# Optimization experiments

Measured on AMD Instinct MI355X. Metric: run time of the kernel, lower is better.

The kernel has to match this reference:

```python
import jax, jax.numpy as jnp
import numpy as np

DIM = 1024
EPS = 1e-5

def layernorm(x, g, b):
    m = jnp.mean(x, axis=-1, keepdims=True)
    v = jnp.var(x, axis=-1, keepdims=True)
    return (x - m) / jnp.sqrt(v + EPS) * g + b

def setup_inputs() -> dict:
    key = jax.random.key(0)
    ks = jax.random.split(key, 12)
    B, L, D = 4, 2048, DIM
    s = 1.0 / np.sqrt(D)
    return {
        "q": jax.random.normal(ks[0], (B, L, D), jnp.float32),
        "k": jax.random.normal(ks[1], (B, L, D), jnp.float32),
        "v": jax.random.normal(ks[2], (B, L, D), jnp.float32),
        "gq": jnp.ones((D,), jnp.float32), "bq": jnp.zeros((D,), jnp.float32),
        "gk": jnp.ones((D,), jnp.float32), "bk": jnp.zeros((D,), jnp.float32),
        "gv": jnp.ones((D,), jnp.float32), "bv": jnp.zeros((D,), jnp.float32),
        "Wq": jax.random.uniform(ks[3], (D, D), jnp.float32, -s, s),
        "Wk": jax.random.uniform(ks[4], (D, D), jnp.float32, -s, s),
        "Wv": jax.random.uniform(ks[5], (D, D), jnp.float32, -s, s),
        "Wp": jax.random.uniform(ks[6], (D, D), jnp.float32, -s, s),
        "bp": jax.random.uniform(ks[7], (D,), jnp.float32, -s, s),
    }

def reference(q, k, v, gq, bq, gk, bk, gv, bv, Wq, Wk, Wv, Wp, bp):
    scale = DIM ** -0.5
    qn = layernorm(q, gq, bq) @ Wq.T  # [B,Q,D]
    kn = layernorm(k, gk, bk) @ Wk.T  # [B,K,D]
    vn = layernorm(v, gv, bv) @ Wv.T  # [B,K,D]
    attn = jnp.einsum('bqc,bkc->bqk', qn, kn)
    attn = jax.nn.relu(attn) * scale  # ReLU on raw scores, then scale (matches in-place *=)
    attn_mask = jax.nn.softmax(attn, axis=-1)
    out = jnp.einsum('bqk,bkc->bqc', attn_mask, vn)
    out = out @ Wp.T + bp
    return (attn, out)
```

## Files before the change

kernel.cpp:

```cpp
#include <hip/hip_runtime.h>


typedef __attribute__((ext_vector_type(8))) short short8v;
typedef __attribute__((ext_vector_type(4))) float f32x4;

#define DEVI __device__ __forceinline__

DEVI float b2f(unsigned short u) {
  union { unsigned int i; float f; } x;
  x.i = ((unsigned int)u) << 16;
  return x.f;
}
DEVI unsigned short f2b(float f) {
  union { float f; unsigned int i; } x;
  x.f = f;
  unsigned int r = x.i + 0x7fffu + ((x.i >> 16) & 1u);
  return (unsigned short)(r >> 16);
}

DEVI bool sniff_bf16(const unsigned short* wq) {
  int bad = 0;
#pragma unroll
  for (int j = 0; j < 64; ++j) bad |= (fabsf(b2f(wq[j])) > 0.0625f) ? 1 : 0;
  return bad == 0;
}

DEVI void async16(const unsigned short* g, unsigned short* l) {
  __builtin_amdgcn_global_load_lds(
      (const __attribute__((address_space(1))) void*)g,
      (__attribute__((address_space(3))) void*)l, 16, 0, 0);
}

DEVI void wait_lgkm0() { asm volatile("s_waitcnt lgkmcnt(0)" ::: "memory"); }
template <int N> DEVI void wait_vm();
template <> DEVI void wait_vm<0>() { asm volatile("s_waitcnt vmcnt(0)" ::: "memory"); }
template <> DEVI void wait_vm<6>() { asm volatile("s_waitcnt vmcnt(6)" ::: "memory"); }
template <> DEVI void wait_vm<8>() { asm volatile("s_waitcnt vmcnt(8)" ::: "memory"); }

DEVI void stage_q(const unsigned short* G, int ld, unsigned short* L,
                  int w, int lane, int k0) {
  int r8 = lane >> 3;
  int scol = ((lane & 7) ^ r8) * 8;
  async16(G + (size_t)(w * 8 + r8) * ld + k0 + scol, L + (w * 8) * 64);
}
DEVI void stage_half(const unsigned short* G, int ld, unsigned short* L,
                     int w, int lane, int k0) {
  stage_q(G, ld, L, w, lane, k0);
  stage_q(G + (size_t)64 * ld, ld, L + 64 * 64, w, lane, k0);
}

template <int NB>
DEVI void gemm8_core(unsigned short* sA, unsigned short* sB,
                     const unsigned short* Ab, const unsigned short* Bb,
                     int m0, int n0, int lda, int ldb, int K, int tid,
                     f32x4 (&acc)[8][2 * NB]) {
  int lane = tid & 63, w = tid >> 6;
  int wm = w >> 2, wn = w & 3;
  int l15 = lane & 15, quad = lane >> 4;
  int rxor = l15 & 7;
  int cb0 = (quad ^ rxor) * 8;
  int cb1 = ((4 + quad) ^ rxor) * 8;
  const int nst = K >> 6;
  const int BSZ = NB * 128 * 64;
  const unsigned short* A_ = Ab + (size_t)m0 * lda;
  const unsigned short* B_ = Bb + (size_t)n0 * ldb;

  if constexpr (NB == 2) {
    stage_half(A_, lda, sA, w, lane, 0);
    stage_half(A_ + (size_t)128 * lda, lda, sA + 8192, w, lane, 0);
    stage_half(B_, ldb, sB, w, lane, 0);
    stage_half(B_ + (size_t)128 * ldb, ldb, sB + 8192, w, lane, 0);
    if (nst > 1) {
      stage_half(A_, lda, sA + 16384, w, lane, 64);
      stage_half(A_ + (size_t)128 * lda, lda, sA + 16384 + 8192, w, lane, 64);
    }
    for (int t = 0; t < nst; ++t) {
      const int b = t & 1;
      const unsigned short* rA = sA + b * 16384 + (wm * 128 + l15) * 64;
      const unsigned short* rB = sB + b * 16384 + (wn * 64 + l15) * 64;
      short8v a[4][2], bb[4][2];
      if (t + 1 < nst) {
        int kn = (t + 1) << 6;
        stage_half(B_, ldb, sB + (b ^ 1) * 16384, w, lane, kn);
        stage_half(B_ + (size_t)128 * ldb, ldb, sB + (b ^ 1) * 16384 + 8192, w, lane, kn);
        wait_vm<8>();
      } else {
        wait_vm<0>();
      }
      __builtin_amdgcn_s_barrier();
#pragma unroll
      for (int mt = 0; mt < 4; ++mt) {
        a[mt][0] = *(const short8v*)(rA + mt * 1024 + cb0);
        a[mt][1] = *(const short8v*)(rA + mt * 1024 + cb1);
      }
#pragma unroll
      for (int nt = 0; nt < 2; ++nt) {
        bb[nt][0] = *(const short8v*)(rB + nt * 1024 + cb0);
        bb[nt][1] = *(const short8v*)(rB + nt * 1024 + cb1);
      }
      wait_lgkm0();
      __builtin_amdgcn_sched_barrier(0);
      __builtin_amdgcn_s_setprio(1);
#pragma unroll
      for (int mt = 0; mt < 4; ++mt)
#pragma unroll
        for (int nt = 0; nt < 2; ++nt) {
          acc[mt][nt] = __builtin_amdgcn_mfma_f32_16x16x32_bf16(a[mt][0], bb[nt][0], acc[mt][nt], 0, 0, 0);
          acc[mt][nt] = __builtin_amdgcn_mfma_f32_16x16x32_bf16(a[mt][1], bb[nt][1], acc[mt][nt], 0, 0, 0);
        }
      __builtin_amdgcn_s_setprio(0);
      __builtin_amdgcn_s_barrier();
#pragma unroll
      for (int nt = 2; nt < 4; ++nt) {
        bb[nt][0] = *(const short8v*)(rB + nt * 1024 + cb0);
        bb[nt][1] = *(const short8v*)(rB + nt * 1024 + cb1);
      }
      __builtin_amdgcn_s_barrier();
      wait_lgkm0();
      __builtin_amdgcn_sched_barrier(0);
      __builtin_amdgcn_s_setprio(1);
#pragma unroll
      for (int mt = 0; mt < 4; ++mt)
#pragma unroll
        for (int nt = 2; nt < 4; ++nt) {
          acc[mt][nt] = __builtin_amdgcn_mfma_f32_16x16x32_bf16(a[mt][0], bb[nt][0], acc[mt][nt], 0, 0, 0);
          acc[mt][nt] = __builtin_amdgcn_mfma_f32_16x16x32_bf16(a[mt][1], bb[nt][1], acc[mt][nt], 0, 0, 0);
        }
      __builtin_amdgcn_s_setprio(0);
      __builtin_amdgcn_s_barrier();
#pragma unroll
      for (int mt = 0; mt < 4; ++mt) {
        a[mt][0] = *(const short8v*)(rA + (4 + mt) * 1024 + cb0);
        a[mt][1] = *(const short8v*)(rA + (4 + mt) * 1024 + cb1);
      }
      __builtin_amdgcn_s_barrier();
      wait_lgkm0();
      __builtin_amdgcn_sched_barrier(0);
      __builtin_amdgcn_s_setprio(1);
#pragma unroll
      for (int mt = 0; mt < 4; ++mt)
#pragma unroll
        for (int nt = 0; nt < 2; ++nt) {
          acc[4 + mt][nt] = __builtin_amdgcn_mfma_f32_16x16x32_bf16(a[mt][0], bb[nt][0], acc[4 + mt][nt], 0, 0, 0);
          acc[4 + mt][nt] = __builtin_amdgcn_mfma_f32_16x16x32_bf16(a[mt][1], bb[nt][1], acc[4 + mt][nt], 0, 0, 0);
        }
      __builtin_amdgcn_s_setprio(0);
      __builtin_amdgcn_s_barrier();
      if (t + 2 < nst) {
        int kn2 = (t + 2) << 6;
        stage_half(A_, lda, sA + b * 16384, w, lane, kn2);
        stage_half(A_ + (size_t)128 * lda, lda, sA + b * 16384 + 8192, w, lane, kn2);
      }
      __builtin_amdgcn_s_setprio(1);
#pragma unroll
      for (int mt = 0; mt < 4; ++mt)
#pragma unroll
        for (int nt = 2; nt < 4; ++nt) {
          acc[4 + mt][nt] = __builtin_amdgcn_mfma_f32_16x16x32_bf16(a[mt][0], bb[nt][0], acc[4 + mt][nt], 0, 0, 0);
          acc[4 + mt][nt] = __builtin_amdgcn_mfma_f32_16x16x32_bf16(a[mt][1], bb[nt][1], acc[4 + mt][nt], 0, 0, 0);
        }
      __builtin_amdgcn_s_setprio(0);
    }
  } else {
    stage_q(A_, lda, sA, w, lane, 0);
    stage_q(A_ + (size_t)128 * lda, lda, sA + 128 * 64, w, lane, 0);
    stage_half(B_, ldb, sB, w, lane, 0);
    stage_q(A_ + (size_t)64 * lda, lda, sA + 64 * 64, w, lane, 0);
    stage_q(A_ + (size_t)192 * lda, lda, sA + 192 * 64, w, lane, 0);
    if (nst > 1) {
      stage_q(A_, lda, sA + 16384, w, lane, 64);
      stage_q(A_ + (size_t)128 * lda, lda, sA + 16384 + 128 * 64, w, lane, 64);
      stage_half(B_, ldb, sB + BSZ, w, lane, 64);
    }
    for (int t = 0; t < nst; ++t) {
      const int b = t & 1;
      const unsigned short* rA = sA + b * 16384 + (wm * 128 + l15) * 64;
      const unsigned short* rB = sB + b * BSZ + (wn * 32 + l15) * 64;
      short8v a[4][2], bb[2][2];
      if (t + 1 < nst) {
        int kn = (t + 1) << 6;
        stage_q(A_ + (size_t)64 * lda, lda, sA + (b ^ 1) * 16384 + 64 * 64, w, lane, kn);
        stage_q(A_ + (size_t)192 * lda, lda, sA + (b ^ 1) * 16384 + 192 * 64, w, lane, kn);
        wait_vm<6>();
      } else {
        wait_vm<0>();
      }
      __builtin_amdgcn_s_barrier();
#pragma unroll
      for (int mt = 0; mt < 4; ++mt) {
        a[mt][0] = *(const short8v*)(rA + mt * 1024 + cb0);
        a[mt][1] = *(const short8v*)(rA + mt * 1024 + cb1);
      }
#pragma unroll
      for (int nt = 0; nt < 2; ++nt) {
        bb[nt][0] = *(const short8v*)(rB + nt * 1024 + cb0);
        bb[nt][1] = *(const short8v*)(rB + nt * 1024 + cb1);
      }
      wait_lgkm0();
      __builtin_amdgcn_sched_barrier(0);
      __builtin_amdgcn_s_setprio(1);
#pragma unroll
      for (int mt = 0; mt < 4; ++mt)
#pragma unroll
        for (int nt = 0; nt < 2; ++nt) {
          acc[mt][nt] = __builtin_amdgcn_mfma_f32_16x16x32_bf16(a[mt][0], bb[nt][0], acc[mt][nt], 0, 0, 0);
          acc[mt][nt] = __builtin_amdgcn_mfma_f32_16x16x32_bf16(a[mt][1], bb[nt][1], acc[mt][nt], 0, 0, 0);
        }
      __builtin_amdgcn_s_setprio(0);
      __builtin_amdgcn_s_barrier();
#pragma unroll
      for (int mt = 0; mt < 4; ++mt) {
        a[mt][0] = *(const short8v*)(rA + (4 + mt) * 1024 + cb0);
        a[mt][1] = *(const short8v*)(rA + (4 + mt) * 1024 + cb1);
      }
      if (t + 2 < nst) {
        int kn2 = (t + 2) << 6;
        stage_q(A_, lda, sA + b * 16384, w, lane, kn2);
        stage_q(A_ + (size_t)128 * lda, lda, sA + b * 16384 + 128 * 64, w, lane, kn2);
        stage_half(B_, ldb, sB + b * BSZ, w, lane, kn2);
      }
      __builtin_amdgcn_s_barrier();
      wait_lgkm0();
      __builtin_amdgcn_sched_barrier(0);
      __builtin_amdgcn_s_setprio(1);
#pragma unroll
      for (int mt = 0; mt < 4; ++mt)
#pragma unroll
        for (int nt = 0; nt < 2; ++nt) {
          acc[4 + mt][nt] = __builtin_amdgcn_mfma_f32_16x16x32_bf16(a[mt][0], bb[nt][0], acc[4 + mt][nt], 0, 0, 0);
          acc[4 + mt][nt] = __builtin_amdgcn_mfma_f32_16x16x32_bf16(a[mt][1], bb[nt][1], acc[4 + mt][nt], 0, 0, 0);
        }
      __builtin_amdgcn_s_setprio(0);
      __builtin_amdgcn_s_barrier();
    }
  }
}

DEVI int xcd_swz(int f, int nb) { return (f & 7) * (nb >> 3) + (f >> 3); }

struct PrepArgs {
  const void* q; const void* k; const void* v;
  const void* g[3]; const void* b[3];
  const void* W[4];
};

__global__ __launch_bounds__(256) void k_prep(PrepArgs pa,
    unsigned short* __restrict__ Wb, unsigned short* __restrict__ XN) {
  bool isbf = sniff_bf16((const unsigned short*)pa.W[0]);
  int bid = blockIdx.x, tid = threadIdx.x;
  if (bid < 2048) {
    int s = bid >> 9;
    size_t inner = ((size_t)(bid & 511)) * 2048 + (size_t)tid * 8;
    unsigned short* dst = Wb + (size_t)s * 1048576 + inner;
    if (isbf) {
      *(uint4*)dst = *(const uint4*)((const unsigned short*)pa.W[s] + inner);
    } else {
      const float* f = (const float*)pa.W[s] + inner;
      float4 a = *(const float4*)f;
      float4 b = *(const float4*)(f + 4);
      ushort4 o0 = { f2b(a.x), f2b(a.y), f2b(a.z), f2b(a.w) };
      ushort4 o1 = { f2b(b.x), f2b(b.y), f2b(b.z), f2b(b.w) };
      *(ushort4*)dst = o0;
      *(ushort4*)(dst + 4) = o1;
    }
  } else {
    int row = bid - 2048;
    int t = row >> 13;
    size_t r = (size_t)(row & 8191);
    const void* src = (t == 0) ? pa.q : (t == 1) ? pa.k : pa.v;
    float x0, x1, x2, x3;
    if (isbf) {
      ushort4 pk = *(const ushort4*)((const unsigned short*)src + r * 1024 + (size_t)tid * 4);
      x0 = b2f(pk.x); x1 = b2f(pk.y); x2 = b2f(pk.z); x3 = b2f(pk.w);
    } else {
      float4 pk = *(const float4*)((const float*)src + r * 1024 + (size_t)tid * 4);
      x0 = pk.x; x1 = pk.y; x2 = pk.z; x3 = pk.w;
    }
    float s1 = x0 + x1 + x2 + x3;
    float s2 = x0 * x0 + x1 * x1 + x2 * x2 + x3 * x3;
    for (int off = 32; off > 0; off >>= 1) {
      s1 += __shfl_down(s1, off);
      s2 += __shfl_down(s2, off);
    }
    __shared__ float sh[8];
    if ((tid & 63) == 0) { sh[tid >> 6] = s1; sh[4 + (tid >> 6)] = s2; }
    __syncthreads();
    float m  = (sh[0] + sh[1] + sh[2] + sh[3]) * (1.0f / 1024.0f);
    float m2 = (sh[4] + sh[5] + sh[6] + sh[7]) * (1.0f / 1024.0f);
    float rstd = rsqrtf(m2 - m * m + 1e-5f);
    float g0, g1, g2, g3, c0, c1, c2, c3;
    if (isbf) {
      ushort4 gv = *(const ushort4*)((const unsigned short*)pa.g[t] + tid * 4);
      ushort4 bbv = *(const ushort4*)((const unsigned short*)pa.b[t] + tid * 4);
      g0 = b2f(gv.x); g1 = b2f(gv.y); g2 = b2f(gv.z); g3 = b2f(gv.w);
      c0 = b2f(bbv.x); c1 = b2f(bbv.y); c2 = b2f(bbv.z); c3 = b2f(bbv.w);
    } else {
      float4 gv = *(const float4*)((const float*)pa.g[t] + tid * 4);
      float4 bbv = *(const float4*)((const float*)pa.b[t] + tid * 4);
      g0 = gv.x; g1 = gv.y; g2 = gv.z; g3 = gv.w;
      c0 = bbv.x; c1 = bbv.y; c2 = bbv.z; c3 = bbv.w;
    }
    ushort4 o;
    o.x = f2b((x0 - m) * rstd * g0 + c0);
    o.y = f2b((x1 - m) * rstd * g1 + c1);
    o.z = f2b((x2 - m) * rstd * g2 + c2);
    o.w = f2b((x3 - m) * rstd * g3 + c3);
    *(ushort4*)(XN + (size_t)row * 1024 + (size_t)tid * 4) = o;
  }
}

__global__ __launch_bounds__(512, 2) void k_megaproj(
    const unsigned short* __restrict__ XN, const unsigned short* __restrict__ Wb,
    unsigned short* __restrict__ QN, unsigned short* __restrict__ VNT) {
  __shared__ __align__(16) unsigned short sA[2 * 256 * 64];
  __shared__ __align__(16) unsigned short sB[2 * 256 * 64];
  int x = xcd_swz((int)blockIdx.x, 384), tid = threadIdx.x;
  int lane = tid & 63, w = tid >> 6;
  int wm = w >> 2, wn = w & 3;
  int l15 = lane & 15, quad = lane >> 4;
  f32x4 acc[8][4];
#pragma unroll
  for (int i = 0; i < 8; ++i)
#pragma unroll
    for (int j = 0; j < 4; ++j) acc[i][j] = (f32x4){0.f, 0.f, 0.f, 0.f};

  unsigned short* C;
  int m0, n0, ldc;
  if (x < 256) {
    int t = x >> 7, i = x & 127;
    m0 = (i >> 2) * 256; n0 = (i & 3) * 256; ldc = 1024;
    gemm8_core<2>(sA, sB, XN + (size_t)t * 8388608, Wb + (size_t)t * 1048576,
                  m0, n0, 1024, 1024, 1024, tid, acc);
    C = QN + (size_t)t * 8388608;
  } else {
    int i = x - 256, z = i >> 5, j = i & 31;
    m0 = (j >> 3) * 256; n0 = (j & 7) * 256; ldc = 2048;
    gemm8_core<2>(sA, sB, Wb + 2 * 1048576, XN + 2 * 8388608 + (size_t)z * 2097152,
                  m0, n0, 1024, 1024, 1024, tid, acc);
    C = VNT + (size_t)z * 2097152;
  }
#pragma unroll
  for (int mt = 0; mt < 8; ++mt) {
    int mb = m0 + wm * 128 + mt * 16 + quad * 4;
#pragma unroll
    for (int nt = 0; nt < 4; ++nt) {
      int n = n0 + wn * 64 + nt * 16 + l15;
      f32x4 vc = acc[mt][nt];
#pragma unroll
      for (int r2 = 0; r2 < 4; ++r2) C[(size_t)(mb + r2) * ldc + n] = f2b(vc[r2]);
    }
  }
}

template <int EPI, int NB>
__global__ __launch_bounds__(512, 2) void k_gemm(
    const unsigned short* __restrict__ A, const unsigned short* __restrict__ B,
    void* __restrict__ Cv, long long coff,
    int K, int lda, int ldb, int ldc,
    long long sAb, long long sBb, long long sCb,
    float scale, const void* __restrict__ bias,
    const unsigned short* __restrict__ wq_sniff) {
  __shared__ __align__(16) unsigned short sA[2 * 256 * 64];
  __shared__ __align__(16) unsigned short sB[2 * NB * 128 * 64];
  int tid = threadIdx.x;
  int lane = tid & 63, w = tid >> 6;
  int wm = w >> 2, wn = w & 3;
  int l15 = lane & 15, quad = lane >> 4;

  int gx = gridDim.x, gy = gridDim.y;
  int nb = gx * gy * (int)gridDim.z;
  int f = (int)blockIdx.x + gx * ((int)blockIdx.y + gy * (int)blockIdx.z);
  f = xcd_swz(f, nb);
  int bx = f % gx;
  int rem = f / gx;
  int by = rem % gy;
  int bz = rem / gy;

  int m0 = by * 256, n0 = bx * (NB * 128);
  f32x4 acc[8][2 * NB];
#pragma unroll
  for (int i = 0; i < 8; ++i)
#pragma unroll
    for (int j = 0; j < 2 * NB; ++j) acc[i][j] = (f32x4){0.f, 0.f, 0.f, 0.f};

  gemm8_core<NB>(sA, sB, A + (long long)bz * sAb, B + (long long)bz * sBb,
                 m0, n0, lda, ldb, K, tid, acc);

  long long cbase = coff + (long long)bz * sCb;
  bool isbf = (EPI != 0) ? sniff_bf16(wq_sniff) : true;
#pragma unroll
  for (int mt = 0; mt < 8; ++mt) {
    int mb = m0 + wm * 128 + mt * 16 + quad * 4;
#pragma unroll
    for (int nt = 0; nt < 2 * NB; ++nt) {
      int n = n0 + wn * (NB * 32) + nt * 16 + l15;
      f32x4 vc = acc[mt][nt];
      if (EPI == 0) {
        unsigned short* C = (unsigned short*)Cv + cbase;
#pragma unroll
        for (int r2 = 0; r2 < 4; ++r2) C[(size_t)(mb + r2) * ldc + n] = f2b(vc[r2]);
      } else if (EPI == 1) {
        if (isbf) {
          unsigned short* C = (unsigned short*)Cv + cbase;
#pragma unroll
          for (int r2 = 0; r2 < 4; ++r2)
            C[(size_t)(mb + r2) * ldc + n] = f2b(fmaxf(vc[r2], 0.f) * scale);
        } else {
          float* C = (float*)Cv + cbase;
#pragma unroll
          for (int r2 = 0; r2 < 4; ++r2)
            C[(size_t)(mb + r2) * ldc + n] = fmaxf(vc[r2], 0.f) * scale;
        }
      } else {
        float bv2 = isbf ? b2f(((const unsigned short*)bias)[n])
                         : ((const float*)bias)[n];
        if (isbf) {
          unsigned short* C = (unsigned short*)Cv + cbase;
#pragma unroll
          for (int r2 = 0; r2 < 4; ++r2) C[(size_t)(mb + r2) * ldc + n] = f2b(vc[r2] + bv2);
        } else {
          float* C = (float*)Cv + cbase;
#pragma unroll
          for (int r2 = 0; r2 < 4; ++r2) C[(size_t)(mb + r2) * ldc + n] = vc[r2] + bv2;
        }
      }
    }
  }
}

__global__ __launch_bounds__(256) void k_softmax(const void* __restrict__ S,
    unsigned short* __restrict__ P, const unsigned short* __restrict__ wq_sniff) {
  bool isbf = sniff_bf16(wq_sniff);
  size_t row = blockIdx.x;
  int tid = threadIdx.x;
  float v[8];
  if (isbf) {
    const unsigned short* s = (const unsigned short*)S + row * 2048 + (size_t)tid * 8;
    ushort4 a = *(const ushort4*)s;
    ushort4 b = *(const ushort4*)(s + 4);
    v[0] = b2f(a.x); v[1] = b2f(a.y); v[2] = b2f(a.z); v[3] = b2f(a.w);
    v[4] = b2f(b.x); v[5] = b2f(b.y); v[6] = b2f(b.z); v[7] = b2f(b.w);
  } else {
    const float* s = (const float*)S + row * 2048 + (size_t)tid * 8;
    float4 a = *(const float4*)s;
    float4 b = *(const float4*)(s + 4);
    v[0] = a.x; v[1] = a.y; v[2] = a.z; v[3] = a.w;
    v[4] = b.x; v[5] = b.y; v[6] = b.z; v[7] = b.w;
  }
  float mx = v[0];
#pragma unroll
  for (int j = 1; j < 8; ++j) mx = fmaxf(mx, v[j]);
  for (int off = 32; off > 0; off >>= 1) mx = fmaxf(mx, __shfl_down(mx, off));
  __shared__ float sh[8];
  if ((tid & 63) == 0) sh[tid >> 6] = mx;
  __syncthreads();
  mx = fmaxf(fmaxf(sh[0], sh[1]), fmaxf(sh[2], sh[3]));
  float sum = 0.f;
#pragma unroll
  for (int j = 0; j < 8; ++j) { v[j] = __expf(v[j] - mx); sum += v[j]; }
  for (int off = 32; off > 0; off >>= 1) sum += __shfl_down(sum, off);
  if ((tid & 63) == 0) sh[4 + (tid >> 6)] = sum;
  __syncthreads();
  float inv = 1.0f / (sh[4] + sh[5] + sh[6] + sh[7]);
  ushort4 o0 = { f2b(v[0] * inv), f2b(v[1] * inv), f2b(v[2] * inv), f2b(v[3] * inv) };
  ushort4 o1 = { f2b(v[4] * inv), f2b(v[5] * inv), f2b(v[6] * inv), f2b(v[7] * inv) };
  unsigned short* p = P + row * 2048 + (size_t)tid * 8;
  *(ushort4*)p = o0;
  *(ushort4*)(p + 4) = o1;
}

static const size_t MB_ = 1024 * 1024;
static const size_t OFF_W   = 0;
static const size_t OFF_XN  = 8 * MB_ + 128 * 1024;
static const size_t OFF_QN  = OFF_XN + 48 * MB_;
static const size_t OFF_VNT = OFF_QN + 32 * MB_;
static const size_t OFF_P   = OFF_XN;
static const size_t OFF_O1  = OFF_XN + 32 * MB_;

extern "C" void kernel_launch(void* const* d_in, const int* in_sizes, int n_in,
                              void* d_out, int out_size, void* d_ws, size_t ws_size,
                              hipStream_t stream) {
  (void)in_sizes; (void)n_in; (void)out_size; (void)ws_size;
  char* ws = (char*)d_ws;
  unsigned short* Wb  = (unsigned short*)(ws + OFF_W);
  unsigned short* XN  = (unsigned short*)(ws + OFF_XN);
  unsigned short* QN  = (unsigned short*)(ws + OFF_QN);
  unsigned short* VNT = (unsigned short*)(ws + OFF_VNT);
  unsigned short* P   = (unsigned short*)(ws + OFF_P);
  unsigned short* O1  = (unsigned short*)(ws + OFF_O1);
  const unsigned short* WqS = (const unsigned short*)d_in[9];

  PrepArgs pa;
  pa.q = d_in[0]; pa.k = d_in[1]; pa.v = d_in[2];
  pa.g[0] = d_in[3]; pa.b[0] = d_in[4];
  pa.g[1] = d_in[5]; pa.b[1] = d_in[6];
  pa.g[2] = d_in[7]; pa.b[2] = d_in[8];
  pa.W[0] = d_in[9]; pa.W[1] = d_in[10]; pa.W[2] = d_in[11]; pa.W[3] = d_in[12];

  k_prep<<<26624, 256, 0, stream>>>(pa, Wb, XN);

  k_megaproj<<<384, 512, 0, stream>>>(XN, Wb, QN, VNT);

  k_gemm<1, 2><<<dim3(8, 8, 4), 512, 0, stream>>>(
      QN, QN + 8388608, d_out,
      0,
      1024, 1024, 1024, 2048,
      2097152LL, 2097152LL, 4194304LL,
      0.03125f, nullptr, WqS);

  k_softmax<<<8192, 256, 0, stream>>>(d_out, P, WqS);

  k_gemm<0, 1><<<dim3(8, 8, 4), 512, 0, stream>>>(
      P, VNT, O1,
      0,
      2048, 2048, 2048, 1024,
      4194304LL, 2097152LL, 2097152LL,
      0.f, nullptr, WqS);

  k_gemm<3, 1><<<dim3(8, 32, 1), 512, 0, stream>>>(
      O1, Wb + 3 * 1048576, d_out,
      16777216,
      1024, 1024, 1024, 1024,
      0LL, 0LL, 0LL,
      0.f, d_in[13], WqS);
}
```

Measured before the change: 414.1 us.

## Re-pipeline NB=2 GEMM staging and use one wave per layernorm row

The NB=2 GEMM main loop is reordered so the A and B half-tiles for later k-steps are issued in finer pieces spread across the four MFMA phases. The register fragments are also split into a03/a47/b01/b23 so each LDS read feeds a quadrant of MFMAs, aiming to hide global-to-LDS latency behind compute. Separately, the layernorm part of k_prep now handles one row per wavefront, 16 elements per lane, using only shuffle reductions. This drops the shared-memory/syncthreads reduction and cuts the grid from 26624 to 8192 blocks. The new vmcnt/lgkmcnt wait counts are delicate and could leave a race if the in-flight load counts do not match.

```diff
diff --git a/kernel.cpp b/kernel.cpp
--- a/kernel.cpp
+++ b/kernel.cpp
@@ -32,10 +32,10 @@
 }
 
 DEVI void wait_lgkm0() { asm volatile("s_waitcnt lgkmcnt(0)" ::: "memory"); }
+DEVI void wait_lgkm8() { asm volatile("s_waitcnt lgkmcnt(8)" ::: "memory"); }
 template <int N> DEVI void wait_vm();
 template <> DEVI void wait_vm<0>() { asm volatile("s_waitcnt vmcnt(0)" ::: "memory"); }
 template <> DEVI void wait_vm<6>() { asm volatile("s_waitcnt vmcnt(6)" ::: "memory"); }
-template <> DEVI void wait_vm<8>() { asm volatile("s_waitcnt vmcnt(8)" ::: "memory"); }
 
 DEVI void stage_q(const unsigned short* G, int ld, unsigned short* L,
                   int w, int lane, int k0) {
@@ -66,38 +66,44 @@
   const unsigned short* B_ = Bb + (size_t)n0 * ldb;
 
   if constexpr (NB == 2) {
-    stage_half(A_, lda, sA, w, lane, 0);
-    stage_half(A_ + (size_t)128 * lda, lda, sA + 8192, w, lane, 0);
-    stage_half(B_, ldb, sB, w, lane, 0);
-    stage_half(B_ + (size_t)128 * ldb, ldb, sB + 8192, w, lane, 0);
+    const unsigned short* A0 = A_;
+    const unsigned short* A1 = A_ + (size_t)128 * lda;
+    const unsigned short* B0g = B_;
+    const unsigned short* B1g = B_ + (size_t)128 * ldb;
+    stage_half(A0, lda, sA, w, lane, 0);
+    stage_half(A1, lda, sA + 8192, w, lane, 0);
+    stage_half(B0g, ldb, sB, w, lane, 0);
+    stage_half(B1g, ldb, sB + 8192, w, lane, 0);
     if (nst > 1) {
-      stage_half(A_, lda, sA + 16384, w, lane, 64);
-      stage_half(A_ + (size_t)128 * lda, lda, sA + 16384 + 8192, w, lane, 64);
-    }
+      stage_half(A0, lda, sA + 16384, w, lane, 64);
+      stage_half(A1, lda, sA + 16384 + 8192, w, lane, 64);
+      stage_half(B0g, ldb, sB + 16384, w, lane, 64);
+      wait_vm<6>();
+    } else {
+      wait_vm<0>();
+    }
+    __builtin_amdgcn_s_barrier();
+
     for (int t = 0; t < nst; ++t) {
-      const int b = t & 1;
+      const int b = t & 1, nb2 = b ^ 1;
       const unsigned short* rA = sA + b * 16384 + (wm * 128 + l15) * 64;
       const unsigned short* rB = sB + b * 16384 + (wn * 64 + l15) * 64;
-      short8v a[4][2], bb[4][2];
-      if (t + 1 < nst) {
-        int kn = (t + 1) << 6;
-        stage_half(B_, ldb, sB + (b ^ 1) * 16384, w, lane, kn);
-        stage_half(B_ + (size_t)128 * ldb, ldb, sB + (b ^ 1) * 16384 + 8192, w, lane, kn);
-        wait_vm<8>();
-      } else {
-        wait_vm<0>();
-      }
-      __builtin_amdgcn_s_barrier();
+      short8v a03[4][2], a47[4][2], b01[2][2], b23[2][2];
+
 #pragma unroll
       for (int mt = 0; mt < 4; ++mt) {
-        a[mt][0] = *(const short8v*)(rA + mt * 1024 + cb0);
-        a[mt][1] = *(const short8v*)(rA + mt * 1024 + cb1);
+        a03[mt][0] = *(const short8v*)(rA + mt * 1024 + cb0);
+        a03[mt][1] = *(const short8v*)(rA + mt * 1024 + cb1);
       }
 #pragma unroll
       for (int nt = 0; nt < 2; ++nt) {
-        bb[nt][0] = *(const short8v*)(rB + nt * 1024 + cb0);
-        bb[nt][1] = *(const short8v*)(rB + nt * 1024 + cb1);
-      }
+        b01[nt][0] = *(const short8v*)(rB + nt * 1024 + cb0);
+        b01[nt][1] = *(const short8v*)(rB + nt * 1024 + cb1);
+      }
+      if (t + 1 < nst)
+        stage_half(B1g, ldb, sB + nb2 * 16384 + 8192, w, lane, (t + 1) << 6);
+      wait_lgkm8();
+      __builtin_amdgcn_s_barrier();
       wait_lgkm0();
       __builtin_amdgcn_sched_barrier(0);
       __builtin_amdgcn_s_setprio(1);
@@ -105,15 +111,16 @@
       for (int mt = 0; mt < 4; ++mt)
 #pragma unroll
         for (int nt = 0; nt < 2; ++nt) {
-          acc[mt][nt] = __builtin_amdgcn_mfma_f32_16x16x32_bf16(a[mt][0], bb[nt][0], acc[mt][nt], 0, 0, 0);
-          acc[mt][nt] = __builtin_amdgcn_mfma_f32_16x16x32_bf16(a[mt][1], bb[nt][1], acc[mt][nt], 0, 0, 0);
+          acc[mt][nt] = __builtin_amdgcn_mfma_f32_16x16x32_bf16(a03[mt][0], b01[nt][0], acc[mt][nt], 0, 0, 0);
+          acc[mt][nt] = __builtin_amdgcn_mfma_f32_16x16x32_bf16(a03[mt][1], b01[nt][1], acc[mt][nt], 0, 0, 0);
         }
       __builtin_amdgcn_s_setprio(0);
       __builtin_amdgcn_s_barrier();
-#pragma unroll
-      for (int nt = 2; nt < 4; ++nt) {
-        bb[nt][0] = *(const short8v*)(rB + nt * 1024 + cb0);
-        bb[nt][1] = *(const short8v*)(rB + nt * 1024 + cb1);
+
+#pragma unroll
+      for (int mt = 0; mt < 4; ++mt) {
+        a47[mt][0] = *(const short8v*)(rA + (4 + mt) * 1024 + cb0);
+        a47[mt][1] = *(const short8v*)(rA + (4 + mt) * 1024 + cb1);
       }
       __builtin_amdgcn_s_barrier();
       wait_lgkm0();
@@ -122,17 +129,20 @@
 #pragma unroll
       for (int mt = 0; mt < 4; ++mt)
 #pragma unroll
-        for (int nt = 2; nt < 4; ++nt) {
-          acc[mt][nt] = __builtin_amdgcn_mfma_f32_16x16x32_bf16(a[mt][0], bb[nt][0], acc[mt][nt], 0, 0, 0);
-          acc[mt][nt] = __builtin_amdgcn_mfma_f32_16x16x32_bf16(a[mt][1], bb[nt][1], acc[mt][nt], 0, 0, 0);
+        for (int nt = 0; nt < 2; ++nt) {
+          acc[4 + mt][nt] = __builtin_amdgcn_mfma_f32_16x16x32_bf16(a47[mt][0], b01[nt][0], acc[4 + mt][nt], 0, 0, 0);
+          acc[4 + mt][nt] = __builtin_amdgcn_mfma_f32_16x16x32_bf16(a47[mt][1], b01[nt][1], acc[4 + mt][nt], 0, 0, 0);
         }
       __builtin_amdgcn_s_setprio(0);
       __builtin_amdgcn_s_barrier();
-#pragma unroll
-      for (int mt = 0; mt < 4; ++mt) {
-        a[mt][0] = *(const short8v*)(rA + (4 + mt) * 1024 + cb0);
-        a[mt][1] = *(const short8v*)(rA + (4 + mt) * 1024 + cb1);
-      }
+
+#pragma unroll
+      for (int nt = 0; nt < 2; ++nt) {
+        b23[nt][0] = *(const short8v*)(rB + (2 + nt) * 1024 + cb0);
+        b23[nt][1] = *(const short8v*)(rB + (2 + nt) * 1024 + cb1);
+      }
+      if (t + 2 < nst)
+        stage_half(A0, lda, sA + b * 16384, w, lane, (t + 2) << 6);
       __builtin_amdgcn_s_barrier();
       wait_lgkm0();
       __builtin_amdgcn_sched_barrier(0);
@@ -141,25 +151,28 @@
       for (int mt = 0; mt < 4; ++mt)
 #pragma unroll
         for (int nt = 0; nt < 2; ++nt) {
-          acc[4 + mt][nt] = __builtin_amdgcn_mfma_f32_16x16x32_bf16(a[mt][0], bb[nt][0], acc[4 + mt][nt], 0, 0, 0);
-          acc[4 + mt][nt] = __builtin_amdgcn_mfma_f32_16x16x32_bf16(a[mt][1], bb[nt][1], acc[4 + mt][nt], 0, 0, 0);
+          acc[mt][2 + nt] = __builtin_amdgcn_mfma_f32_16x16x32_bf16(a03[mt][0], b23[nt][0], acc[mt][2 + nt], 0, 0, 0);
+          acc[mt][2 + nt] = __builtin_amdgcn_mfma_f32_16x16x32_bf16(a03[mt][1], b23[nt][1], acc[mt][2 + nt], 0, 0, 0);
         }
       __builtin_amdgcn_s_setprio(0);
       __builtin_amdgcn_s_barrier();
+
       if (t + 2 < nst) {
-        int kn2 = (t + 2) << 6;
-        stage_half(A_, lda, sA + b * 16384, w, lane, kn2);
-        stage_half(A_ + (size_t)128 * lda, lda, sA + b * 16384 + 8192, w, lane, kn2);
+        stage_half(A1, lda, sA + b * 16384 + 8192, w, lane, (t + 2) << 6);
+        stage_half(B0g, ldb, sB + b * 16384, w, lane, (t + 2) << 6);
       }
       __builtin_amdgcn_s_setprio(1);
 #pragma unroll
       for (int mt = 0; mt < 4; ++mt)
 #pragma unroll
-        for (int nt = 2; nt < 4; ++nt) {
-          acc[4 + mt][nt] = __builtin_amdgcn_mfma_f32_16x16x32_bf16(a[mt][0], bb[nt][0], acc[4 + mt][nt], 0, 0, 0);
-          acc[4 + mt][nt] = __builtin_amdgcn_mfma_f32_16x16x32_bf16(a[mt][1], bb[nt][1], acc[4 + mt][nt], 0, 0, 0);
+        for (int nt = 0; nt < 2; ++nt) {
+          acc[4 + mt][2 + nt] = __builtin_amdgcn_mfma_f32_16x16x32_bf16(a47[mt][0], b23[nt][0], acc[4 + mt][2 + nt], 0, 0, 0);
+          acc[4 + mt][2 + nt] = __builtin_amdgcn_mfma_f32_16x16x32_bf16(a47[mt][1], b23[nt][1], acc[4 + mt][2 + nt], 0, 0, 0);
         }
       __builtin_amdgcn_s_setprio(0);
+      if (t + 2 < nst) wait_vm<6>();
+      else if (t + 1 < nst) wait_vm<0>();
+      __builtin_amdgcn_s_barrier();
     }
   } else {
     stage_q(A_, lda, sA, w, lane, 0);
@@ -264,48 +277,73 @@
       *(ushort4*)(dst + 4) = o1;
     }
   } else {
-    int row = bid - 2048;
+    int rb = bid - 2048;
+    int wv = tid >> 6, lane = tid & 63;
+    int row = rb * 4 + wv;
     int t = row >> 13;
     size_t r = (size_t)(row & 8191);
     const void* src = (t == 0) ? pa.q : (t == 1) ? pa.k : pa.v;
-    float x0, x1, x2, x3;
+    float x[16];
     if (isbf) {
-      ushort4 pk = *(const ushort4*)((const unsigned short*)src + r * 1024 + (size_t)tid * 4);
-      x0 = b2f(pk.x); x1 = b2f(pk.y); x2 = b2f(pk.z); x3 = b2f(pk.w);
+      const unsigned short* s = (const unsigned short*)src + r * 1024;
+#pragma unroll
+      for (int j = 0; j < 2; ++j) {
+        uint4 pk = *(const uint4*)(s + j * 512 + lane * 8);
+        const unsigned short* ps = (const unsigned short*)&pk;
+#pragma unroll
+        for (int e = 0; e < 8; ++e) x[j * 8 + e] = b2f(ps[e]);
+      }
     } else {
-      float4 pk = *(const float4*)((const float*)src + r * 1024 + (size_t)tid * 4);
-      x0 = pk.x; x1 = pk.y; x2 = pk.z; x3 = pk.w;
-    }
-    float s1 = x0 + x1 + x2 + x3;
-    float s2 = x0 * x0 + x1 * x1 + x2 * x2 + x3 * x3;
+      const float* s = (const float*)src + r * 1024;
+#pragma unroll
+      for (int j = 0; j < 4; ++j) {
+        float4 pk = *(const float4*)(s + j * 256 + lane * 4);
+        x[j * 4 + 0] = pk.x; x[j * 4 + 1] = pk.y;
+        x[j * 4 + 2] = pk.z; x[j * 4 + 3] = pk.w;
+      }
+    }
+    float s1 = 0.f, s2 = 0.f;
+#pragma unroll
+    for (int e = 0; e < 16; ++e) { s1 += x[e]; s2 += x[e] * x[e]; }
     for (int off = 32; off > 0; off >>= 1) {
-      s1 += __shfl_down(s1, off);
-      s2 += __shfl_down(s2, off);
-    }
-    __shared__ float sh[8];
-    if ((tid & 63) == 0) { sh[tid >> 6] = s1; sh[4 + (tid >> 6)] = s2; }
-    __syncthreads();
-    float m  = (sh[0] + sh[1] + sh[2] + sh[3]) * (1.0f / 1024.0f);
-    float m2 = (sh[4] + sh[5] + sh[6] + sh[7]) * (1.0f / 1024.0f);
+      s1 += __shfl_xor(s1, off);
+      s2 += __shfl_xor(s2, off);
+    }
+    float m  = s1 * (1.0f / 1024.0f);
+    float m2 = s2 * (1.0f / 1024.0f);
     float rstd = rsqrtf(m2 - m * m + 1e-5f);
-    float g0, g1, g2, g3, c0, c1, c2, c3;
+    unsigned short* dst = XN + (size_t)row * 1024;
     if (isbf) {
-      ushort4 gv = *(const ushort4*)((const unsigned short*)pa.g[t] + tid * 4);
-      ushort4 bbv = *(const ushort4*)((const unsigned short*)pa.b[t] + tid * 4);
-      g0 = b2f(gv.x); g1 = b2f(gv.y); g2 = b2f(gv.z); g3 = b2f(gv.w);
-      c0 = b2f(bbv.x); c1 = b2f(bbv.y); c2 = b2f(bbv.z); c3 = b2f(bbv.w);
+      const unsigned short* gp = (const unsigned short*)pa.g[t];
+      const unsigned short* bp = (const unsigned short*)pa.b[t];
+#pragma unroll
+      for (int j = 0; j < 2; ++j) {
+        uint4 gk = *(const uint4*)(gp + j * 512 + lane * 8);
+        uint4 bk = *(const uint4*)(bp + j * 512 + lane * 8);
+        const unsigned short* gs = (const unsigned short*)&gk;
+        const unsigned short* bs = (const unsigned short*)&bk;
+        uint4 out;
+        unsigned short* os = (unsigned short*)&out;
+#pragma unroll
+        for (int e = 0; e < 8; ++e)
+          os[e] = f2b((x[j * 8 + e] - m) * rstd * b2f(gs[e]) + b2f(bs[e]));
+        *(uint4*)(dst + j * 512 + lane * 8) = out;
+      }
     } else {
-      float4 gv = *(const float4*)((const float*)pa.g[t] + tid * 4);
-      float4 bbv = *(const float4*)((const float*)pa.b[t] + tid * 4);
-      g0 = gv.x; g1 = gv.y; g2 = gv.z; g3 = gv.w;
-      c0 = bbv.x; c1 = bbv.y; c2 = bbv.z; c3 = bbv.w;
-    }
-    ushort4 o;
-    o.x = f2b((x0 - m) * rstd * g0 + c0);
-    o.y = f2b((x1 - m) * rstd * g1 + c1);
-    o.z = f2b((x2 - m) * rstd * g2 + c2);
-    o.w = f2b((x3 - m) * rstd * g3 + c3);
-    *(ushort4*)(XN + (size_t)row * 1024 + (size_t)tid * 4) = o;
+      const float* gp = (const float*)pa.g[t];
+      const float* bp = (const float*)pa.b[t];
+#pragma unroll
+      for (int j = 0; j < 4; ++j) {
+        float4 gk = *(const float4*)(gp + j * 256 + lane * 4);
+        float4 bk = *(const float4*)(bp + j * 256 + lane * 4);
+        ushort4 o;
+        o.x = f2b((x[j * 4 + 0] - m) * rstd * gk.x + bk.x);
+        o.y = f2b((x[j * 4 + 1] - m) * rstd * gk.y + bk.y);
+        o.z = f2b((x[j * 4 + 2] - m) * rstd * gk.z + bk.z);
+        o.w = f2b((x[j * 4 + 3] - m) * rstd * gk.w + bk.w);
+        *(ushort4*)(dst + j * 256 + lane * 4) = o;
+      }
+    }
   }
 }
 
@@ -497,7 +535,7 @@
   pa.g[2] = d_in[7]; pa.b[2] = d_in[8];
   pa.W[0] = d_in[9]; pa.W[1] = d_in[10]; pa.W[2] = d_in[11]; pa.W[3] = d_in[12];
 
-  k_prep<<<26624, 256, 0, stream>>>(pa, Wb, XN);
+  k_prep<<<8192, 256, 0, stream>>>(pa, Wb, XN);
 
   k_megaproj<<<384, 512, 0, stream>>>(XN, Wb, QN, VNT);
 
```

Result: faster. 404.4 us (-2.3%).
